# Kernel optimization log

Measured on AMD Instinct MI355X. Metric: run time of the kernel, lower is better.

The kernel has to match this reference:

```python
import jax, jax.numpy as jnp
from jax import lax
import numpy as np

B, C_IN, L = 8, 256, 2048
NUM_SPKS = 2
N_MAMBA = 2          # n_layers - 1
D_STATE = 16
D_CONV = 4
EXPAND = 2
D_INNER = EXPAND * C_IN            # 512
DT_RANK = (C_IN + 15) // 16        # 16 (mamba_ssm default ceil(d_model/16))


def setup_inputs() -> dict:
    key = jax.random.key(0)
    ks = jax.random.split(key, 16)
    s = 0.02
    inp = {
        "input": jax.random.normal(ks[0], (B, C_IN, L), jnp.float32),
        # stacked per-layer Mamba params, leading dim = N_MAMBA
        "in_proj_w": jax.random.normal(ks[1], (N_MAMBA, 2 * D_INNER, C_IN), jnp.float32) * s,
        "conv_w": jax.random.normal(ks[2], (N_MAMBA, D_INNER, 1, D_CONV), jnp.float32) * s,
        "conv_b": jnp.zeros((N_MAMBA, D_INNER), jnp.float32),
        "x_proj_w": jax.random.normal(ks[3], (N_MAMBA, DT_RANK + 2 * D_STATE, D_INNER), jnp.float32) * s,
        "dt_proj_w": jax.random.normal(ks[4], (N_MAMBA, D_INNER, DT_RANK), jnp.float32) * s,
        "dt_proj_b": jax.random.normal(ks[5], (N_MAMBA, D_INNER), jnp.float32) * 0.1,
        "A_log": jnp.tile(jnp.log(jnp.arange(1, D_STATE + 1, dtype=jnp.float32))[None, None, :],
                          (N_MAMBA, D_INNER, 1)),
        "D": jnp.ones((N_MAMBA, D_INNER), jnp.float32),
        "out_proj_w": jax.random.normal(ks[6], (N_MAMBA, C_IN, D_INNER), jnp.float32) * s,
        "out_lin_w": jax.random.normal(ks[7], (NUM_SPKS * C_IN, C_IN), jnp.float32) * s,
        "out_lin_b": jnp.zeros((NUM_SPKS * C_IN,), jnp.float32),
    }
    return inp


def _mamba_layer(x, in_proj_w, conv_w, conv_b, x_proj_w, dt_proj_w, dt_proj_b, A_log, Dp, out_proj_w):
    # x: [B, L, C_IN]
    xz = jnp.einsum('blc,ec->ble', x, in_proj_w)          # [B, L, 2*D_INNER]
    xr, z = jnp.split(xz, 2, axis=-1)
    # causal depthwise conv1d over time
    xc = lax.conv_general_dilated(
        xr.transpose(0, 2, 1), conv_w, window_strides=(1,),
        padding=[(D_CONV - 1, 0)], feature_group_count=D_INNER,
        dimension_numbers=('NCH', 'OIH', 'NCH'))
    xc = jax.nn.silu(xc + conv_b[None, :, None]).transpose(0, 2, 1)  # [B, L, D_INNER]
    # input-dependent SSM params
    x_db = jnp.einsum('bld,ed->ble', xc, x_proj_w)        # [B, L, DT_RANK + 2*D_STATE]
    dt = x_db[..., :DT_RANK]
    Bm = x_db[..., DT_RANK:DT_RANK + D_STATE]             # [B, L, D_STATE]
    Cm = x_db[..., DT_RANK + D_STATE:]                    # [B, L, D_STATE]
    delta = jax.nn.softplus(jnp.einsum('blr,dr->bld', dt, dt_proj_w) + dt_proj_b)  # [B, L, D_INNER]
    A = -jnp.exp(A_log)                                   # [D_INNER, D_STATE]

    def step(h, inp):
        d_t, b_t, c_t, x_t = inp                          # [B,Din],[B,Ds],[B,Ds],[B,Din]
        dA = jnp.exp(d_t[:, :, None] * A)                 # [B, Din, Ds]
        h = dA * h + (d_t * x_t)[:, :, None] * b_t[:, None, :]
        y = jnp.einsum('bds,bs->bd', h, c_t)
        return h, y

    xs = (delta.transpose(1, 0, 2), Bm.transpose(1, 0, 2),
          Cm.transpose(1, 0, 2), xc.transpose(1, 0, 2))
    h0 = jnp.zeros((x.shape[0], D_INNER, D_STATE), x.dtype)
    _, ys = lax.scan(step, h0, xs)                        # ys: [L, B, D_INNER]
    y = ys.transpose(1, 0, 2) + xc * Dp                   # skip term D*x
    y = y * jax.nn.silu(z)
    return jnp.einsum('bld,cd->blc', y, out_proj_w)       # [B, L, C_IN]


def reference(input, in_proj_w, conv_w, conv_b, x_proj_w, dt_proj_w, dt_proj_b,
              A_log, D, out_proj_w, out_lin_w, out_lin_b):
    out = input.transpose(0, 2, 1)                        # movedim(-1,-2): [B, L, C]
    for i in range(N_MAMBA):
        out = _mamba_layer(out, in_proj_w[i], conv_w[i], conv_b[i], x_proj_w[i],
                           dt_proj_w[i], dt_proj_b[i], A_log[i], D[i], out_proj_w[i])
    out = jnp.einsum('blc,oc->blo', out, out_lin_w) + out_lin_b
    out = jax.nn.relu(out)                                # [B, L, NUM_SPKS*C]
    Bb, Ll, _ = out.shape
    out = out.transpose(2, 0, 1).reshape(NUM_SPKS, C_IN, Bb, Ll)
    return out.transpose(0, 2, 1, 3)                      # [NUM_SPKS, B, C, L]
```

## Files before the change

kernel.cpp:

```cpp
#include <hip/hip_runtime.h>
#include <cmath>

#define L_SEQ 2048
#define BATCH 8
#define CIN 256
#define DIN 512
#define M_ROWS (BATCH * L_SEQ)
#define NC 64
#define LC 32

typedef __attribute__((ext_vector_type(8))) short short8;
typedef __attribute__((ext_vector_type(4))) unsigned short ushort4v;
typedef __attribute__((ext_vector_type(4))) float float4v;
typedef unsigned short u16;

__device__ inline u16 f2bf_rn(float x) {
  union { float f; unsigned u; } v;
  v.f = x;
  unsigned r = v.u + 0x7FFF + ((v.u >> 16) & 1);
  return (u16)(r >> 16);
}
__device__ inline float bf2f(u16 h) {
  union { unsigned u; float f; } v;
  v.u = ((unsigned)h) << 16;
  return v.f;
}

__device__ inline void gl_lds16(const u16* g, u16* l) {
  __builtin_amdgcn_global_load_lds(
      (const __attribute__((address_space(1))) unsigned int*)(const void*)g,
      (__attribute__((address_space(3))) unsigned int*)(void*)l, 16, 0, 0);
}

__global__ __launch_bounds__(256) void transpose_in(const float* __restrict__ in,
                                                    u16* __restrict__ xh, u16* __restrict__ xl) {
  __shared__ float tile[32][33];
  int b = blockIdx.z;
  int l0 = blockIdx.x * 32, c0 = blockIdx.y * 32;
  int tx = threadIdx.x, ty = threadIdx.y;
#pragma unroll
  for (int k = 0; k < 4; ++k)
    tile[ty + k * 8][tx] = in[(long)(b * CIN + c0 + ty + k * 8) * L_SEQ + l0 + tx];
  __syncthreads();
#pragma unroll
  for (int k = 0; k < 4; ++k) {
    float v = tile[tx][ty + k * 8];
    long o = (long)(b * L_SEQ + l0 + ty + k * 8) * CIN + c0 + tx;
    u16 h = f2bf_rn(v);
    xh[o] = h;
    xl[o] = f2bf_rn(v - bf2f(h));
  }
}

__global__ __launch_bounds__(256) void split_pack(const float* __restrict__ in,
                                                  u16* __restrict__ oh, u16* __restrict__ ol,
                                                  int n) {
  int i = blockIdx.x * 256 + threadIdx.x;
  if (i < n) {
    float v = in[i];
    u16 h = f2bf_rn(v);
    oh[i] = h;
    ol[i] = f2bf_rn(v - bf2f(h));
  }
}

__global__ __launch_bounds__(256) void build_wd(const float* __restrict__ xpw,
                                                const float* __restrict__ dtw,
                                                u16* __restrict__ Wh, u16* __restrict__ Wl) {
  int k = blockIdx.x * 256 + threadIdx.x;
  int n = blockIdx.y;
  float v;
  if (n < 512) {
    v = 0.f;
#pragma unroll
    for (int r = 0; r < 16; ++r) v += dtw[n * 16 + r] * xpw[r * 512 + k];
  } else if (n < 544) {
    v = xpw[(16 + n - 512) * 512 + k];
  } else {
    v = 0.f;
  }
  u16 h = f2bf_rn(v);
  Wh[(long)n * 512 + k] = h;
  Wl[(long)n * 512 + k] = f2bf_rn(v - bf2f(h));
}

__global__ __launch_bounds__(256) void build_wcomb(const float* __restrict__ olw,
                                                   const float* __restrict__ opw,
                                                   u16* __restrict__ Wh, u16* __restrict__ Wl) {
  int d = blockIdx.x * 256 + threadIdx.x;
  int o = blockIdx.y;
  float v = 0.f;
#pragma unroll 4
  for (int c = 0; c < 256; ++c) v += olw[o * 256 + c] * opw[(long)c * 512 + d];
  u16 h = f2bf_rn(v);
  Wh[(long)o * 512 + d] = h;
  Wl[(long)o * 512 + d] = f2bf_rn(v - bf2f(h));
}

template <int EPI, int NBN>
__global__ __launch_bounds__(256) void gemm_mfma(const u16* __restrict__ Ahp,
                                                 const u16* __restrict__ Alp, int lda,
                                                 const u16* __restrict__ Whp,
                                                 const u16* __restrict__ Wlp, int K,
                                                 float* __restrict__ C, float* __restrict__ C2,
                                                 u16* __restrict__ Ch, u16* __restrict__ Cl,
                                                 u16* __restrict__ Ch2, u16* __restrict__ Cl2,
                                                 const float* __restrict__ bias) {
  __shared__ u16 Ah[128 * 32], Al[128 * 32];
  __shared__ u16 Wh[64 * 32], Wl[64 * 32];
  int g = blockIdx.x;
  int bm = (g & 7) * 16 + (g >> 3) / NBN;
  int bn = (g >> 3) % NBN;
  long m0 = (long)bm * 128, n0 = (long)bn * 64;
  int tid = threadIdx.x;
  int w = tid >> 6, L = tid & 63;
  int q = L >> 4, r16 = L & 15;
  int wm = (w >> 1) * 64, wn = (w & 1) * 32;
  float4v acc[4][2];
#pragma unroll
  for (int i = 0; i < 4; ++i)
#pragma unroll
    for (int j = 0; j < 2; ++j) acc[i][j] = (float4v){0.f, 0.f, 0.f, 0.f};

  int lrow = L >> 2;
  int lcol = (((L & 3) - (L >> 3)) & 3) * 8;
  int rchunk = (q + (r16 >> 1)) & 3;

  for (int k0 = 0; k0 < K; k0 += 32) {
#pragma unroll
    for (int is = 0; is < 2; ++is) {
      int chunk = w + is * 4;
      int row = chunk * 16 + lrow;
      long ga = (m0 + row) * (long)lda + k0 + lcol;
      gl_lds16(&Ahp[ga], &Ah[chunk * 512]);
      gl_lds16(&Alp[ga], &Al[chunk * 512]);
    }
    {
      int row = w * 16 + lrow;
      long gw = (n0 + row) * (long)K + k0 + lcol;
      gl_lds16(&Whp[gw], &Wh[w * 512]);
      gl_lds16(&Wlp[gw], &Wl[w * 512]);
    }
    __syncthreads();
    short8 ah[4], al[4], bh[2], bl[2];
#pragma unroll
    for (int i = 0; i < 4; ++i) {
      int mr = wm + i * 16 + r16;
      ah[i] = *(const short8*)&Ah[mr * 32 + rchunk * 8];
      al[i] = *(const short8*)&Al[mr * 32 + rchunk * 8];
    }
#pragma unroll
    for (int j = 0; j < 2; ++j) {
      int nr = wn + j * 16 + r16;
      bh[j] = *(const short8*)&Wh[nr * 32 + rchunk * 8];
      bl[j] = *(const short8*)&Wl[nr * 32 + rchunk * 8];
    }
#pragma unroll
    for (int i = 0; i < 4; ++i)
#pragma unroll
      for (int j = 0; j < 2; ++j) {
        acc[i][j] = __builtin_amdgcn_mfma_f32_16x16x32_bf16(ah[i], bh[j], acc[i][j], 0, 0, 0);
        acc[i][j] = __builtin_amdgcn_mfma_f32_16x16x32_bf16(al[i], bh[j], acc[i][j], 0, 0, 0);
        acc[i][j] = __builtin_amdgcn_mfma_f32_16x16x32_bf16(ah[i], bl[j], acc[i][j], 0, 0, 0);
      }
    __syncthreads();
  }

#pragma unroll
  for (int i = 0; i < 4; ++i) {
    int m = (int)m0 + wm + i * 16 + q * 4;
#pragma unroll
    for (int j = 0; j < 2; ++j) {
      int n = (int)n0 + wn + j * 16 + r16;
      if (EPI == 3) {
        u16* dh = (n < 512) ? Ch : Ch2;
        u16* dl = (n < 512) ? Cl : Cl2;
        int nn = n & 511;
#pragma unroll
        for (int r = 0; r < 4; ++r) {
          float v = acc[i][j][r];
          u16 h = f2bf_rn(v);
          dh[(long)(m + r) * 512 + nn] = h;
          dl[(long)(m + r) * 512 + nn] = f2bf_rn(v - bf2f(h));
        }
      } else if (EPI == 4) {
        if (n < 512) {
          float vb = bias[n];
#pragma unroll
          for (int r = 0; r < 4; ++r) {
            float t = acc[i][j][r] + vb;
            t = (t > 20.f) ? t : __logf(1.f + __expf(t));
            u16 h = f2bf_rn(t);
            Ch[(long)(m + r) * 512 + n] = h;
            Cl[(long)(m + r) * 512 + n] = f2bf_rn(t - bf2f(h));
          }
        } else if (n < 544) {
#pragma unroll
          for (int r = 0; r < 4; ++r) C2[(long)(m + r) * 32 + (n - 512)] = acc[i][j][r];
        }
      } else if (EPI == 5) {
#pragma unroll
        for (int r = 0; r < 4; ++r) {
          float v = acc[i][j][r];
          u16 h = f2bf_rn(v);
          Ch[(long)(m + r) * 256 + n] = h;
          Cl[(long)(m + r) * 256 + n] = f2bf_rn(v - bf2f(h));
        }
      } else {
        float vb = bias[n];
        int spk = n >> 8, c = n & 255;
        int b = m >> 11, l = m & 2047;
        float4v v;
#pragma unroll
        for (int r = 0; r < 4; ++r) {
          float t = acc[i][j][r] + vb;
          v[r] = t > 0.f ? t : 0.f;
        }
        *(float4v*)&C[(((long)(spk * BATCH + b)) * CIN + c) * L_SEQ + l] = v;
      }
    }
  }
}

__global__ __launch_bounds__(256) void conv_silu(const u16* __restrict__ xrh,
                                                 const u16* __restrict__ xrl,
                                                 const float* __restrict__ cw,
                                                 const float* __restrict__ cb,
                                                 u16* __restrict__ xch, u16* __restrict__ xcl) {
  int tid = threadIdx.x;
  int d = (tid & 127) * 4;
  int r0 = blockIdx.x * 32 + (tid >> 7) * 16;
  float4v wv[4];
#pragma unroll
  for (int e = 0; e < 4; ++e) wv[e] = *(const float4v*)&cw[(d + e) * 4];
  float4v bias4 = *(const float4v*)&cb[d];
  float4v x0 = {0.f, 0.f, 0.f, 0.f}, x1 = x0, x2 = x0, x3;
  if ((r0 & 2047) != 0) {
#pragma unroll
    for (int p = 0; p < 3; ++p) {
      long row = (long)(r0 - 3 + p) * 512 + d;
      ushort4v hh = *(const ushort4v*)&xrh[row];
      ushort4v ll = *(const ushort4v*)&xrl[row];
      float4v xv;
#pragma unroll
      for (int e = 0; e < 4; ++e) xv[e] = bf2f(hh[e]) + bf2f(ll[e]);
      if (p == 0) x0 = xv;
      else if (p == 1) x1 = xv;
      else x2 = xv;
    }
  }
#pragma unroll 4
  for (int t = 0; t < 16; ++t) {
    long row = (long)(r0 + t) * 512 + d;
    ushort4v hh = *(const ushort4v*)&xrh[row];
    ushort4v ll = *(const ushort4v*)&xrl[row];
#pragma unroll
    for (int e = 0; e < 4; ++e) x3[e] = bf2f(hh[e]) + bf2f(ll[e]);
    ushort4v oh, ol;
#pragma unroll
    for (int e = 0; e < 4; ++e) {
      float a = bias4[e] + wv[e][0] * x0[e] + wv[e][1] * x1[e] + wv[e][2] * x2[e] +
                wv[e][3] * x3[e];
      float v = a / (1.f + __expf(-a));
      u16 h = f2bf_rn(v);
      oh[e] = h;
      ol[e] = f2bf_rn(v - bf2f(h));
    }
    *(ushort4v*)&xch[row] = oh;
    *(ushort4v*)&xcl[row] = ol;
    x0 = x1;
    x1 = x2;
    x2 = x3;
  }
}

__global__ __launch_bounds__(256) void scan_pass1(const u16* __restrict__ dh,
                                                  const u16* __restrict__ dl,
                                                  const u16* __restrict__ xch,
                                                  const u16* __restrict__ xcl,
                                                  const float* __restrict__ bc,
                                                  const float* __restrict__ A_log,
                                                  float* __restrict__ P,
                                                  float* __restrict__ Hl) {
  int b = blockIdx.z, c = blockIdx.y;
  int tid = threadIdx.x;
  int d = blockIdx.x * 256 + tid;
  __shared__ float sBC[LC][32];
  const long base = (long)b * L_SEQ + (long)c * LC;
  ((float4v*)sBC)[tid] = ((const float4v*)&bc[base * 32])[tid];
  float Aval[16];
  {
    float4v a[4];
#pragma unroll
    for (int g = 0; g < 4; ++g) a[g] = *(const float4v*)&A_log[d * 16 + g * 4];
#pragma unroll
    for (int s = 0; s < 16; ++s) Aval[s] = -__expf(a[s >> 2][s & 3]);
  }
  __syncthreads();
  float h[16];
#pragma unroll
  for (int s = 0; s < 16; ++s) h[s] = 0.f;
  float sd = 0.f;
#pragma unroll 4
  for (int t = 0; t < LC; ++t) {
    long off = (base + t) * 512 + d;
    float dlv = bf2f(dh[off]) + bf2f(dl[off]);
    float xv = bf2f(xch[off]) + bf2f(xcl[off]);
    float w = dlv * xv;
    sd += dlv;
    float4v Bv[4];
#pragma unroll
    for (int g = 0; g < 4; ++g) Bv[g] = *(const float4v*)&sBC[t][g * 4];
#pragma unroll
    for (int s = 0; s < 16; ++s) {
      float dA = __expf(dlv * Aval[s]);
      h[s] = dA * h[s] + w * Bv[s >> 2][s & 3];
    }
  }
  long idx = (((long)b * NC + c) * 512 + d) * 16;
#pragma unroll
  for (int g = 0; g < 4; ++g) {
    float4v pv, hv;
#pragma unroll
    for (int e = 0; e < 4; ++e) {
      pv[e] = __expf(Aval[g * 4 + e] * sd);
      hv[e] = h[g * 4 + e];
    }
    *(float4v*)&P[idx + g * 4] = pv;
    *(float4v*)&Hl[idx + g * 4] = hv;
  }
}

__global__ __launch_bounds__(256) void scan_combine(const float* __restrict__ P,
                                                    const float* __restrict__ Hl,
                                                    float* __restrict__ H0) {
  int idx = blockIdx.x * 256 + threadIdx.x;
  int b = idx >> 13;
  int ds = idx & 8191;
  float h = 0.f;
#pragma unroll 8
  for (int c = 0; c < NC; ++c) {
    long off = (((long)b * NC + c) << 13) + ds;
    H0[off] = h;
    h = P[off] * h + Hl[off];
  }
}

__global__ __launch_bounds__(256) void scan_pass2(const u16* __restrict__ dh,
                                                  const u16* __restrict__ dl,
                                                  u16* __restrict__ yh, u16* __restrict__ yl,
                                                  const u16* __restrict__ xch,
                                                  const u16* __restrict__ xcl,
                                                  const float* __restrict__ bc,
                                                  const u16* __restrict__ zh,
                                                  const u16* __restrict__ zl,
                                                  const float* __restrict__ A_log,
                                                  const float* __restrict__ Dp,
                                                  const float* __restrict__ H0) {
  int b = blockIdx.z, c = blockIdx.y;
  int tid = threadIdx.x;
  int d = blockIdx.x * 256 + tid;
  __shared__ float sBC[LC][32];
  const long base = (long)b * L_SEQ + (long)c * LC;
  ((float4v*)sBC)[tid] = ((const float4v*)&bc[base * 32])[tid];
  float Aval[16];
  {
    float4v a[4];
#pragma unroll
    for (int g = 0; g < 4; ++g) a[g] = *(const float4v*)&A_log[d * 16 + g * 4];
#pragma unroll
    for (int s = 0; s < 16; ++s) Aval[s] = -__expf(a[s >> 2][s & 3]);
  }
  float Dval = Dp[d];
  float h[16];
  {
    long hidx = (((long)b * NC + c) * 512 + d) * 16;
#pragma unroll
    for (int g = 0; g < 4; ++g) {
      float4v hv = *(const float4v*)&H0[hidx + g * 4];
#pragma unroll
      for (int e = 0; e < 4; ++e) h[g * 4 + e] = hv[e];
    }
  }
  __syncthreads();
#pragma unroll 4
  for (int t = 0; t < LC; ++t) {
    long off = (base + t) * 512 + d;
    float dlv = bf2f(dh[off]) + bf2f(dl[off]);
    float xv = bf2f(xch[off]) + bf2f(xcl[off]);
    float zv = bf2f(zh[off]) + bf2f(zl[off]);
    float w = dlv * xv;
    float4v Bv[4], Cv[4];
#pragma unroll
    for (int g = 0; g < 4; ++g) {
      Bv[g] = *(const float4v*)&sBC[t][g * 4];
      Cv[g] = *(const float4v*)&sBC[t][16 + g * 4];
    }
    float ya = 0.f, yb = 0.f, yc2 = 0.f, yd = 0.f;
#pragma unroll
    for (int s = 0; s < 4; ++s) {
      float dA = __expf(dlv * Aval[s]);
      h[s] = dA * h[s] + w * Bv[0][s];
      ya += h[s] * Cv[0][s];
    }
#pragma unroll
    for (int s = 4; s < 8; ++s) {
      float dA = __expf(dlv * Aval[s]);
      h[s] = dA * h[s] + w * Bv[1][s - 4];
      yb += h[s] * Cv[1][s - 4];
    }
#pragma unroll
    for (int s = 8; s < 12; ++s) {
      float dA = __expf(dlv * Aval[s]);
      h[s] = dA * h[s] + w * Bv[2][s - 8];
      yc2 += h[s] * Cv[2][s - 8];
    }
#pragma unroll
    for (int s = 12; s < 16; ++s) {
      float dA = __expf(dlv * Aval[s]);
      h[s] = dA * h[s] + w * Bv[3][s - 12];
      yd += h[s] * Cv[3][s - 12];
    }
    float yv = (ya + yb) + (yc2 + yd);
    float yf = (yv + xv * Dval) * (zv / (1.f + __expf(-zv)));
    u16 hh = f2bf_rn(yf);
    yh[off] = hh;
    yl[off] = f2bf_rn(yf - bf2f(hh));
  }
}

extern "C" void kernel_launch(void* const* d_in, const int* in_sizes, int n_in, void* d_out,
                              int out_size, void* d_ws, size_t ws_size, hipStream_t stream) {
  const float* input = (const float*)d_in[0];
  const float* in_proj_w = (const float*)d_in[1];
  const float* conv_w = (const float*)d_in[2];
  const float* conv_b = (const float*)d_in[3];
  const float* x_proj_w = (const float*)d_in[4];
  const float* dt_proj_w = (const float*)d_in[5];
  const float* dt_proj_b = (const float*)d_in[6];
  const float* A_log = (const float*)d_in[7];
  const float* Dp = (const float*)d_in[8];
  const float* out_proj_w = (const float*)d_in[9];
  const float* out_lin_w = (const float*)d_in[10];
  const float* out_lin_b = (const float*)d_in[11];

  char* ws = (char*)d_ws;
  u16* buf_xh = (u16*)(ws);
  u16* buf_xl = (u16*)(ws + 8388608);
  u16* buf_xrh = (u16*)(ws + 16777216);
  u16* buf_xrl = (u16*)(ws + 33554432);
  u16* buf_zh = (u16*)(ws + 50331648);
  u16* buf_zl = (u16*)(ws + 67108864);
  u16* buf_xch = (u16*)(ws + 83886080);
  u16* buf_xcl = (u16*)(ws + 100663296);
  float* buf_bc = (float*)(ws + 117440512);
  u16* buf_wch = (u16*)(ws + 119537664);
  u16* buf_wcl = (u16*)(ws + 120061952);
  u16* buf_dh = (u16*)(ws + 120586240);
  u16* buf_dl = (u16*)(ws + 137363456);
  u16* buf_wd0h = (u16*)(ws + 154140672);
  u16* buf_wd0l = (u16*)(ws + 154796032);
  u16* buf_wd1h = (u16*)(ws + 155451392);
  u16* buf_wd1l = (u16*)(ws + 156106752);
  u16* buf_wth = (u16*)(ws + 156762112);
  u16* buf_wtl = (u16*)(ws + 157286400);
  float* buf_P = (float*)(ws + 16777216);
  float* buf_Hl = (float*)(ws + 33554432);
  float* buf_H0 = (float*)ws;
  u16* buf_yh = (u16*)(ws + 16777216);
  u16* buf_yl = (u16*)(ws + 33554432);

  build_wd<<<dim3(2, 576), 256, 0, stream>>>(x_proj_w, dt_proj_w, buf_wd0h, buf_wd0l);
  build_wd<<<dim3(2, 576), 256, 0, stream>>>(x_proj_w + 48 * 512, dt_proj_w + 512 * 16, buf_wd1h,
                                             buf_wd1l);
  build_wcomb<<<dim3(2, 512), 256, 0, stream>>>(out_lin_w, out_proj_w + (long)256 * 512, buf_wch,
                                                buf_wcl);
  transpose_in<<<dim3(64, 8, 8), dim3(32, 8), 0, stream>>>(input, buf_xh, buf_xl);

  for (int i = 0; i < 2; ++i) {
    split_pack<<<1024, 256, 0, stream>>>(in_proj_w + (long)i * 1024 * 256, buf_wth, buf_wtl,
                                         1024 * 256);
    gemm_mfma<3, 16><<<2048, 256, 0, stream>>>(buf_xh, buf_xl, 256, buf_wth, buf_wtl, 256,
                                               nullptr, nullptr, buf_xrh, buf_xrl, buf_zh,
                                               buf_zl, nullptr);
    conv_silu<<<512, 256, 0, stream>>>(buf_xrh, buf_xrl, conv_w + i * 512 * 4, conv_b + i * 512,
                                       buf_xch, buf_xcl);
    gemm_mfma<4, 9><<<1152, 256, 0, stream>>>(
        buf_xch, buf_xcl, 512, (i == 0) ? buf_wd0h : buf_wd1h, (i == 0) ? buf_wd0l : buf_wd1l,
        512, nullptr, buf_bc, buf_dh, buf_dl, nullptr, nullptr, dt_proj_b + i * 512);
    scan_pass1<<<dim3(2, NC, 8), 256, 0, stream>>>(buf_dh, buf_dl, buf_xch, buf_xcl, buf_bc,
                                                   A_log + (long)i * 512 * 16, buf_P, buf_Hl);
    scan_combine<<<256, 256, 0, stream>>>(buf_P, buf_Hl, buf_H0);
    scan_pass2<<<dim3(2, NC, 8), 256, 0, stream>>>(buf_dh, buf_dl, buf_yh, buf_yl, buf_xch,
                                                   buf_xcl, buf_bc, buf_zh, buf_zl,
                                                   A_log + (long)i * 512 * 16, Dp + i * 512,
                                                   buf_H0);
    if (i == 0) {
      split_pack<<<512, 256, 0, stream>>>(out_proj_w, buf_wth, buf_wtl, 256 * 512);
      gemm_mfma<5, 4><<<512, 256, 0, stream>>>(buf_yh, buf_yl, 512, buf_wth, buf_wtl, 512,
                                               nullptr, nullptr, buf_xh, buf_xl, nullptr,
                                               nullptr, nullptr);
    } else {
      gemm_mfma<2, 8><<<1024, 256, 0, stream>>>(buf_yh, buf_yl, 512, buf_wch, buf_wcl, 512,
                                                (float*)d_out, nullptr, nullptr, nullptr,
                                                nullptr, nullptr, out_lin_b);
    }
  }
}
```

Baseline: 557.9 us.

## Double-buffer LDS tiles in split-bf16 MFMA GEMM to overlap loads with compute

After: 577.8 us. 3.6% more time.

```diff
diff --git a/kernel.cpp b/kernel.cpp
--- a/kernel.cpp
+++ b/kernel.cpp
@@ -106,8 +106,8 @@
                                                  u16* __restrict__ Ch, u16* __restrict__ Cl,
                                                  u16* __restrict__ Ch2, u16* __restrict__ Cl2,
                                                  const float* __restrict__ bias) {
-  __shared__ u16 Ah[128 * 32], Al[128 * 32];
-  __shared__ u16 Wh[64 * 32], Wl[64 * 32];
+  __shared__ u16 Ah[2][128 * 32], Al[2][128 * 32];
+  __shared__ u16 Wh[2][64 * 32], Wl[2][64 * 32];
   int g = blockIdx.x;
   int bm = (g & 7) * 16 + (g >> 3) / NBN;
   int bn = (g >> 3) % NBN;
@@ -126,34 +126,45 @@
   int lcol = (((L & 3) - (L >> 3)) & 3) * 8;
   int rchunk = (q + (r16 >> 1)) & 3;
 
-  for (int k0 = 0; k0 < K; k0 += 32) {
-#pragma unroll
-    for (int is = 0; is < 2; ++is) {
-      int chunk = w + is * 4;
-      int row = chunk * 16 + lrow;
-      long ga = (m0 + row) * (long)lda + k0 + lcol;
-      gl_lds16(&Ahp[ga], &Ah[chunk * 512]);
-      gl_lds16(&Alp[ga], &Al[chunk * 512]);
-    }
-    {
-      int row = w * 16 + lrow;
-      long gw = (n0 + row) * (long)K + k0 + lcol;
-      gl_lds16(&Whp[gw], &Wh[w * 512]);
-      gl_lds16(&Wlp[gw], &Wl[w * 512]);
-    }
-    __syncthreads();
+  int nt = K >> 5;
+
+#define STAGE_TILE(kk, bu)                                        \
+  do {                                                            \
+    _Pragma("unroll") for (int is = 0; is < 2; ++is) {            \
+      int chunk = w + is * 4;                                     \
+      int row = chunk * 16 + lrow;                                \
+      long ga = (m0 + row) * (long)lda + (kk) + lcol;             \
+      gl_lds16(&Ahp[ga], &Ah[bu][chunk * 512]);                   \
+      gl_lds16(&Alp[ga], &Al[bu][chunk * 512]);                   \
+    }                                                             \
+    {                                                             \
+      int row = w * 16 + lrow;                                    \
+      long gw = (n0 + row) * (long)K + (kk) + lcol;               \
+      gl_lds16(&Whp[gw], &Wh[bu][w * 512]);                       \
+      gl_lds16(&Wlp[gw], &Wl[bu][w * 512]);                       \
+    }                                                             \
+  } while (0)
+
+  STAGE_TILE(0, 0);
+  asm volatile("s_waitcnt vmcnt(0)" ::: "memory");
+  __builtin_amdgcn_s_barrier();
+  __builtin_amdgcn_sched_barrier(0);
+
+  for (int t = 0; t < nt; ++t) {
+    int cur = t & 1;
+    if (t + 1 < nt) STAGE_TILE((t + 1) << 5, cur ^ 1);
     short8 ah[4], al[4], bh[2], bl[2];
 #pragma unroll
     for (int i = 0; i < 4; ++i) {
       int mr = wm + i * 16 + r16;
-      ah[i] = *(const short8*)&Ah[mr * 32 + rchunk * 8];
-      al[i] = *(const short8*)&Al[mr * 32 + rchunk * 8];
+      ah[i] = *(const short8*)&Ah[cur][mr * 32 + rchunk * 8];
+      al[i] = *(const short8*)&Al[cur][mr * 32 + rchunk * 8];
     }
 #pragma unroll
     for (int j = 0; j < 2; ++j) {
       int nr = wn + j * 16 + r16;
-      bh[j] = *(const short8*)&Wh[nr * 32 + rchunk * 8];
-      bl[j] = *(const short8*)&Wl[nr * 32 + rchunk * 8];
+      bh[j] = *(const short8*)&Wh[cur][nr * 32 + rchunk * 8];
+      bl[j] = *(const short8*)&Wl[cur][nr * 32 + rchunk * 8];
     }
 #pragma unroll
     for (int i = 0; i < 4; ++i)
@@ -163,8 +174,13 @@
         acc[i][j] = __builtin_amdgcn_mfma_f32_16x16x32_bf16(al[i], bh[j], acc[i][j], 0, 0, 0);
         acc[i][j] = __builtin_amdgcn_mfma_f32_16x16x32_bf16(ah[i], bl[j], acc[i][j], 0, 0, 0);
       }
-    __syncthreads();
-  }
+    if (t + 1 < nt) {
+      asm volatile("s_waitcnt vmcnt(0)" ::: "memory");
+      __builtin_amdgcn_s_barrier();
+      __builtin_amdgcn_sched_barrier(0);
+    }
+  }
+#undef STAGE_TILE
 
 #pragma unroll
   for (int i = 0; i < 4; ++i) {
```
